# Performance work log

Hardware: AMD Instinct MI355X
Metric: run time of the kernel (lower is better)

Reference implementation:

```python
import jax, jax.numpy as jnp
import numpy as np
import math

HEAD_DIM = 128
DEPTH = 12
LAMBDA_INIT = 0.8 - 0.6 * math.exp(-0.3 * DEPTH)
EPS = 1e-5
SCALE = 1.0 / math.sqrt(HEAD_DIM / 2)


def setup_inputs() -> dict:
    key = jax.random.key(0)
    ks = jax.random.split(key, 8)
    b, t, d = 2, 4096, 2048
    return {
        "x": jax.random.normal(ks[0], (b, t, d), dtype=jnp.float32),
        "wq": jax.random.normal(ks[1], (d, HEAD_DIM), dtype=jnp.float32) * 0.02,
        "wk": jax.random.normal(ks[2], (d, HEAD_DIM), dtype=jnp.float32) * 0.02,
        "wv": jax.random.normal(ks[3], (d, HEAD_DIM), dtype=jnp.float32) * 0.02,
        "lambda_q1": jax.random.normal(ks[4], (HEAD_DIM // 2,), dtype=jnp.float32) * 0.1,
        "lambda_q2": jax.random.normal(ks[5], (HEAD_DIM // 2,), dtype=jnp.float32) * 0.1,
        "lambda_k1": jax.random.normal(ks[6], (HEAD_DIM // 2,), dtype=jnp.float32) * 0.1,
        "lambda_k2": jax.random.normal(ks[7], (HEAD_DIM // 2,), dtype=jnp.float32) * 0.1,
        "ln_weight": jnp.ones((HEAD_DIM,), dtype=jnp.float32),
    }


def reference(x, wq, wk, wv, lambda_q1, lambda_q2, lambda_k1, lambda_k2, ln_weight):
    b, t, d = x.shape
    q = x @ wq  # [b,t,hd]
    k = x @ wk
    v = x @ wv
    h = HEAD_DIM // 2
    q1, q2 = q[..., :h], q[..., h:]
    k1, k2 = k[..., :h], k[..., h:]
    # causal mask: True where attention is disallowed (strictly upper triangle)
    causal = jnp.triu(jnp.ones((t, t), dtype=bool), k=1)
    neg_inf = jnp.float32(-jnp.inf)

    def masked_softmax(qh, kh):
        scores = jnp.einsum('btd,bsd->bts', qh, kh) * SCALE
        scores = jnp.where(causal, neg_inf, scores)
        return jax.nn.softmax(scores, axis=-1)

    a1 = masked_softmax(q1, k1)
    a2 = masked_softmax(q2, k2)
    lmbda = (jnp.exp(jnp.sum(lambda_q1 * lambda_k1))
             - jnp.exp(jnp.sum(lambda_q2 * lambda_k2))
             + LAMBDA_INIT)
    diffattn = jnp.einsum('bts,bsd->btd', a1 - lmbda * a2, v)
    rms = jnp.sqrt(jnp.mean(diffattn * diffattn, axis=-1, keepdims=True) + EPS)
    out = (1.0 - LAMBDA_INIT) * (diffattn / rms * ln_weight)
    return out
```

## Files before the change

kernel.cpp:

```cpp
#include <hip/hip_runtime.h>
#include <stdint.h>

#define T_SEQ 4096
#define NB 2
#define D_MODEL 2048
#define HD 128

typedef __attribute__((ext_vector_type(4)))  float f32x4;
typedef __attribute__((ext_vector_type(16))) float f32x16;
typedef __attribute__((ext_vector_type(8)))  short bf16x8;
typedef __attribute__((ext_vector_type(4)))  unsigned u32x4;

#define LAMBDA_INIT 0.7836057665316244f
#define OUT_SCALE   0.21639423346837556f

__device__ __forceinline__ unsigned short f2bf(float f) {
  unsigned int u = __float_as_uint(f);
  u += 0x7FFFu + ((u >> 16) & 1u);
  return (unsigned short)(u >> 16);
}
__device__ __forceinline__ float bf2f(unsigned short h) {
  return __uint_as_float(((unsigned int)h) << 16);
}
__device__ __forceinline__ unsigned cvt_pk_bf16(float a, float b) {
  unsigned r;
  asm("v_cvt_pk_bf16_f32 %0, %1, %2" : "=v"(r) : "v"(a), "v"(b));
  return r;
}

__global__ __launch_bounds__(256) void qkv_proj(
    const float* __restrict__ x, const float* __restrict__ wq,
    const float* __restrict__ wk, const float* __restrict__ wv,
    unsigned short* __restrict__ qb, unsigned short* __restrict__ kS,
    unsigned short* __restrict__ vS)
{
  __shared__ __align__(16) unsigned short Ah[64 * 4 * 8];
  __shared__ __align__(16) unsigned short Bh[4 * 132 * 8];
  const int which = blockIdx.y;
  const float* w = (which == 0) ? wq : ((which == 1) ? wk : wv);
  const int m0 = blockIdx.x * 64;
  const int tid = threadIdx.x;
  const int lane = tid & 63, wid = tid >> 6;
  const int wm = wid >> 1, wn = wid & 1;
  const int fr = lane & 15, fq = lane >> 4;

  f32x4 acc[2][4];
  #pragma unroll
  for (int i = 0; i < 2; ++i)
    #pragma unroll
    for (int j = 0; j < 4; ++j) acc[i][j] = (f32x4){0.f, 0.f, 0.f, 0.f};

  f32x4 arg[2], brg[4];
  #pragma unroll
  for (int c = 0; c < 2; ++c) {
    int id = tid + c * 256, r = id >> 3, c4 = (id & 7) << 2;
    arg[c] = *reinterpret_cast<const f32x4*>(&x[(size_t)(m0 + r) * D_MODEL + c4]);
  }
  #pragma unroll
  for (int c = 0; c < 4; ++c) {
    int id = tid + c * 256, n = id & 127, kc = (id >> 7) << 2;
    #pragma unroll
    for (int j = 0; j < 4; ++j) brg[c][j] = w[(size_t)(kc + j) * HD + n];
  }

  for (int it = 0; it < 64; ++it) {
    #pragma unroll
    for (int c = 0; c < 2; ++c) {
      int id = tid + c * 256, r = id >> 3, ac = (id & 7) << 2;
      uint2 ph;
      ph.x = cvt_pk_bf16(arg[c][0], arg[c][1]);
      ph.y = cvt_pk_bf16(arg[c][2], arg[c][3]);
      *reinterpret_cast<uint2*>(&Ah[(r * 4 + (ac >> 3)) * 8 + (ac & 4)]) = ph;
    }
    #pragma unroll
    for (int c = 0; c < 4; ++c) {
      int id = tid + c * 256, n = id & 127, kc = (id >> 7) << 2;
      uint2 ph;
      ph.x = cvt_pk_bf16(brg[c][0], brg[c][1]);
      ph.y = cvt_pk_bf16(brg[c][2], brg[c][3]);
      *reinterpret_cast<uint2*>(&Bh[((kc >> 3) * 132 + n) * 8 + (kc & 4)]) = ph;
    }
    __syncthreads();
    if (it < 63) {
      int k0n = (it + 1) * 32;
      #pragma unroll
      for (int c = 0; c < 2; ++c) {
        int id = tid + c * 256, r = id >> 3, c4 = (id & 7) << 2;
        arg[c] = *reinterpret_cast<const f32x4*>(&x[(size_t)(m0 + r) * D_MODEL + k0n + c4]);
      }
      #pragma unroll
      for (int c = 0; c < 4; ++c) {
        int id = tid + c * 256, n = id & 127, kc = (id >> 7) << 2;
        #pragma unroll
        for (int j = 0; j < 4; ++j) brg[c][j] = w[(size_t)(k0n + kc + j) * HD + n];
      }
    }
    bf16x8 ah[2], bh[4];
    #pragma unroll
    for (int mi = 0; mi < 2; ++mi)
      ah[mi] = *reinterpret_cast<bf16x8*>(&Ah[((wm * 32 + mi * 16 + fr) * 4 + fq) * 8]);
    #pragma unroll
    for (int ni = 0; ni < 4; ++ni)
      bh[ni] = *reinterpret_cast<bf16x8*>(&Bh[(fq * 132 + wn * 64 + ni * 16 + fr) * 8]);
    #pragma unroll
    for (int mi = 0; mi < 2; ++mi)
      #pragma unroll
      for (int ni = 0; ni < 4; ++ni)
        acc[mi][ni] = __builtin_amdgcn_mfma_f32_16x16x32_bf16(ah[mi], bh[ni], acc[mi][ni], 0, 0, 0);
    __syncthreads();
  }
  #pragma unroll
  for (int mi = 0; mi < 2; ++mi)
    #pragma unroll
    for (int ni = 0; ni < 4; ++ni) {
      int n = wn * 64 + ni * 16 + fr;
      #pragma unroll
      for (int r = 0; r < 4; ++r) {
        int m = m0 + wm * 32 + mi * 16 + fq * 4 + r;
        float vv = acc[mi][ni][r];
        int bb = m >> 12, tt = m & 4095;
        int kt = tt >> 5, kvl = tt & 31;
        if (which == 0) {
          qb[(size_t)m * HD + n] = f2bf(vv * 0.125f);
        } else if (which == 1) {
          int g = n >> 6, hl = n & 63;
          int ks = hl >> 4, r8 = (hl >> 3) & 1, e = hl & 7;
          size_t idx = ((((((size_t)bb * 128 + kt) * 2 + g) * 4) + ks) << 9)
                     + (size_t)(kvl + 32 * r8) * 8 + e;
          kS[idx] = f2bf(vv);
        } else {
          int f = kvl >> 4, r8 = (kvl >> 3) & 1, e = kvl & 7;
          int vcb = n >> 5;
          size_t idx = (((((size_t)bb * 128 + kt) * 8) + vcb * 2 + f) << 9)
                     + (size_t)((n & 31) + 32 * r8) * 8 + e;
          vS[idx] = f2bf(vv);
        }
      }
    }
}

template<int LOG2S>
__global__ __launch_bounds__(256, 2) void diff_attn_part(
    const unsigned short* __restrict__ qb, const unsigned short* __restrict__ kS,
    const unsigned short* __restrict__ vS,
    unsigned short* __restrict__ po, float* __restrict__ pm, float* __restrict__ pl)
{
  constexpr int S = 1 << LOG2S;
  const int tid = threadIdx.x, lane = tid & 63, wid = tid >> 6;
  const int wave_id = blockIdx.x * 4 + wid;
  const int sp = wave_id & (S - 1);
  const int g  = (wave_id >> LOG2S) & 1;
  const int qt_raw = (wave_id >> (LOG2S + 1)) & 127;
  const int b  = wave_id >> (LOG2S + 8);
  const int qt = 127 - qt_raw;
  const int slot = (((b * 128 + qt) * 2 + g) << LOG2S) + sp;
  const int lq = lane & 31, lh = lane >> 5;
  const int q0 = qt * 32;
  const int n  = qt + 1;
  const int kt0 = (n * sp) >> LOG2S;
  const int kt1 = (n * (sp + 1)) >> LOG2S;

  bf16x8 qf[4];
  const unsigned short* qp = qb + ((size_t)b * T_SEQ + q0 + lq) * HD + g * 64 + lh * 8;
  #pragma unroll
  for (int ks = 0; ks < 4; ++ks) qf[ks] = *reinterpret_cast<const bf16x8*>(qp + ks * 16);

  f32x16 acc[4];
  #pragma unroll
  for (int v = 0; v < 4; ++v)
    #pragma unroll
    for (int r = 0; r < 16; ++r) acc[v][r] = 0.f;
  float mrun = -1e30f, lrun = 0.f;

  const unsigned short* kbase = kS + ((size_t)(b * 128) * 2 + g) * 4 * 512 + lane * 8;
  const unsigned short* vbase = vS + (size_t)(b * 128) * 8 * 512 + lane * 8;
  #define KFRAG(kt, ks) (kbase + ((size_t)(kt) * 8 + (ks)) * 512)
  #define VFRAG(kt, f)  (vbase + ((size_t)(kt) * 8 + (f)) * 512)

  bf16x8 kf[4];
  if (kt0 < kt1) {
    #pragma unroll
    for (int ks = 0; ks < 4; ++ks)
      kf[ks] = *reinterpret_cast<const bf16x8*>(KFRAG(kt0, ks));
  }

  for (int kt = kt0; kt < kt1; ++kt) {
    bf16x8 vfa[4], vfb[4];
    #pragma unroll
    for (int vcb = 0; vcb < 4; ++vcb) {
      vfa[vcb] = *reinterpret_cast<const bf16x8*>(VFRAG(kt, vcb * 2));
      vfb[vcb] = *reinterpret_cast<const bf16x8*>(VFRAG(kt, vcb * 2 + 1));
    }
    bf16x8 kfn[4];
    const bool more = (kt + 1 < kt1);
    if (more) {
      #pragma unroll
      for (int ks = 0; ks < 4; ++ks)
        kfn[ks] = *reinterpret_cast<const bf16x8*>(KFRAG(kt + 1, ks));
    }
    f32x16 sc;
    #pragma unroll
    for (int r = 0; r < 16; ++r) sc[r] = 0.f;
    #pragma unroll
    for (int ks = 0; ks < 4; ++ks)
      sc = __builtin_amdgcn_mfma_f32_32x32x16_bf16(kf[ks], qf[ks], sc, 0, 0, 0);

    float p[16];
    if (kt == n - 1) {
      #pragma unroll
      for (int r = 0; r < 16; ++r) {
        int rloc = (r & 3) + 8 * (r >> 2) + 4 * lh;
        p[r] = (rloc > lq) ? -1e30f : sc[r];
      }
    } else {
      #pragma unroll
      for (int r = 0; r < 16; ++r) p[r] = sc[r];
    }
    float t16[16];
    #pragma unroll
    for (int r = 0; r < 16; ++r) t16[r] = p[r];
    #pragma unroll
    for (int st = 8; st >= 1; st >>= 1)
      #pragma unroll
      for (int r = 0; r < 8; ++r)
        if (r < st) t16[r] = fmaxf(t16[r], t16[r + st]);
    float pmax = fmaxf(t16[0], __shfl_xor(t16[0], 32));
    if (__any(pmax > mrun + 8.f)) {
      float mn = fmaxf(mrun, pmax);
      float al = __expf(mrun - mn);
      lrun *= al;
      #pragma unroll
      for (int v = 0; v < 4; ++v)
        #pragma unroll
        for (int r = 0; r < 16; ++r) acc[v][r] *= al;
      mrun = mn;
    }
    float psum;
    {
      float s16[16];
      #pragma unroll
      for (int r = 0; r < 16; ++r) { p[r] = __expf(p[r] - mrun); s16[r] = p[r]; }
      #pragma unroll
      for (int st = 8; st >= 1; st >>= 1)
        #pragma unroll
        for (int r = 0; r < 8; ++r)
          if (r < st) s16[r] += s16[r + st];
      psum = s16[0];
    }
    lrun += psum + __shfl_xor(psum, 32);

    unsigned A0 = cvt_pk_bf16(p[0],  p[1]),  A1 = cvt_pk_bf16(p[2],  p[3]);
    unsigned A2 = cvt_pk_bf16(p[4],  p[5]),  A3 = cvt_pk_bf16(p[6],  p[7]);
    unsigned A4 = cvt_pk_bf16(p[8],  p[9]),  A5 = cvt_pk_bf16(p[10], p[11]);
    unsigned A6 = cvt_pk_bf16(p[12], p[13]), A7 = cvt_pk_bf16(p[14], p[15]);
    unsigned pA0 = (unsigned)__shfl_xor((int)A0, 32);
    unsigned pA1 = (unsigned)__shfl_xor((int)A1, 32);
    unsigned pA2 = (unsigned)__shfl_xor((int)A2, 32);
    unsigned pA3 = (unsigned)__shfl_xor((int)A3, 32);
    unsigned pA4 = (unsigned)__shfl_xor((int)A4, 32);
    unsigned pA5 = (unsigned)__shfl_xor((int)A5, 32);
    unsigned pA6 = (unsigned)__shfl_xor((int)A6, 32);
    unsigned pA7 = (unsigned)__shfl_xor((int)A7, 32);
    u32x4 w0, w1;
    w0[0] = lh ? pA2 : A0;  w0[1] = lh ? pA3 : A1;
    w0[2] = lh ? A2  : pA0; w0[3] = lh ? A3  : pA1;
    w1[0] = lh ? pA6 : A4;  w1[1] = lh ? pA7 : A5;
    w1[2] = lh ? A6  : pA4; w1[3] = lh ? A7  : pA5;
    bf16x8 pb0 = *reinterpret_cast<bf16x8*>(&w0);
    bf16x8 pb1 = *reinterpret_cast<bf16x8*>(&w1);
    #pragma unroll
    for (int vcb = 0; vcb < 4; ++vcb) {
      acc[vcb] = __builtin_amdgcn_mfma_f32_32x32x16_bf16(vfa[vcb], pb0, acc[vcb], 0, 0, 0);
      acc[vcb] = __builtin_amdgcn_mfma_f32_32x32x16_bf16(vfb[vcb], pb1, acc[vcb], 0, 0, 0);
    }
    if (more) {
      #pragma unroll
      for (int ks = 0; ks < 4; ++ks) kf[ks] = kfn[ks];
    }
  }
  #undef KFRAG
  #undef VFRAG
  const size_t pbase = (size_t)slot * (HD * 32);
  #pragma unroll
  for (int vcb = 0; vcb < 4; ++vcb)
    #pragma unroll
    for (int r = 0; r < 16; ++r) {
      int vc = vcb * 32 + (r & 3) + 8 * (r >> 2) + 4 * lh;
      po[pbase + (size_t)vc * 32 + lq] = f2bf(acc[vcb][r]);
    }
  if (lane < 32) {
    pm[slot * 32 + lq] = mrun;
    pl[slot * 32 + lq] = lrun;
  }
}

template<int LOG2S>
__global__ __launch_bounds__(256) void diff_merge(
    const unsigned short* __restrict__ po, const float* __restrict__ pm,
    const float* __restrict__ pl,
    const float* __restrict__ lq1, const float* __restrict__ lq2,
    const float* __restrict__ lk1, const float* __restrict__ lk2,
    const float* __restrict__ lnw, float* __restrict__ out)
{
  constexpr int S = 1 << LOG2S;
  __shared__ float red[4][32];
  const int tid = threadIdx.x, lane = tid & 63, wid = tid >> 6;
  const int q = tid & 31, vg = tid >> 5;
  const int bq = blockIdx.x;
  const int b = bq >> 7, qt = bq & 127;

  float la = lq1[lane] * lk1[lane];
  float lb = lq2[lane] * lk2[lane];
  #pragma unroll
  for (int off = 32; off >= 1; off >>= 1) {
    la += __shfl_xor(la, off);
    lb += __shfl_xor(lb, off);
  }
  const float lam = __expf(la) - __expf(lb) + LAMBDA_INIT;

  const int p1 = (bq * 2 + 0) * S;
  const int p2 = (bq * 2 + 1) * S;
  float w1[S], w2[S];
  {
    float ms[S];
    #pragma unroll
    for (int s = 0; s < S; ++s) ms[s] = pm[(p1 + s) * 32 + q];
    float M = ms[0];
    #pragma unroll
    for (int s = 1; s < S; ++s) M = fmaxf(M, ms[s]);
    float L = 0.f;
    #pragma unroll
    for (int s = 0; s < S; ++s) { w1[s] = __expf(ms[s] - M); L += w1[s] * pl[(p1 + s) * 32 + q]; }
    float inv = 1.f / L;
    #pragma unroll
    for (int s = 0; s < S; ++s) w1[s] *= inv;
  }
  {
    float ms[S];
    #pragma unroll
    for (int s = 0; s < S; ++s) ms[s] = pm[(p2 + s) * 32 + q];
    float M = ms[0];
    #pragma unroll
    for (int s = 1; s < S; ++s) M = fmaxf(M, ms[s]);
    float L = 0.f;
    #pragma unroll
    for (int s = 0; s < S; ++s) { w2[s] = __expf(ms[s] - M); L += w2[s] * pl[(p2 + s) * 32 + q]; }
    float inv = lam / L;
    #pragma unroll
    for (int s = 0; s < S; ++s) w2[s] *= inv;
  }
  float d[16], ss = 0.f;
  #pragma unroll
  for (int i = 0; i < 16; ++i) {
    int vc = vg * 16 + i;
    float a1 = 0.f, a2 = 0.f;
    #pragma unroll
    for (int s = 0; s < S; ++s) {
      a1 += w1[s] * bf2f(po[(size_t)(p1 + s) * (HD * 32) + (size_t)vc * 32 + q]);
      a2 += w2[s] * bf2f(po[(size_t)(p2 + s) * (HD * 32) + (size_t)vc * 32 + q]);
    }
    d[i] = a1 - a2;
    ss += d[i] * d[i];
  }
  ss += __shfl_xor(ss, 32);
  if (lane < 32) red[wid][q] = ss;
  __syncthreads();
  float tot = red[0][q] + red[1][q] + red[2][q] + red[3][q];
  float rinv = 1.f / sqrtf(tot * (1.0f / HD) + 1e-5f);
  float* op = out + ((size_t)b * T_SEQ + qt * 32 + q) * HD + vg * 16;
  #pragma unroll
  for (int i = 0; i < 16; ++i) op[i] = OUT_SCALE * d[i] * rinv * lnw[vg * 16 + i];
}

extern "C" void kernel_launch(void* const* d_in, const int* in_sizes, int n_in,
                              void* d_out, int out_size, void* d_ws, size_t ws_size,
                              hipStream_t stream) {
  const float* x   = (const float*)d_in[0];
  const float* wq  = (const float*)d_in[1];
  const float* wk  = (const float*)d_in[2];
  const float* wv  = (const float*)d_in[3];
  const float* lq1 = (const float*)d_in[4];
  const float* lq2 = (const float*)d_in[5];
  const float* lk1 = (const float*)d_in[6];
  const float* lk2 = (const float*)d_in[7];
  const float* lnw = (const float*)d_in[8];
  float* out = (float*)d_out;

  const size_t N = (size_t)NB * T_SEQ * HD;
  int log2S = 3;
  for (; log2S > 0; --log2S) {
    size_t parts = ((size_t)NB * 128 * 2) << log2S;
    size_t need = 3 * N * 2 + parts * (HD * 32) * 2 + parts * 32 * 8;
    if (need <= ws_size) break;
  }
  const size_t parts = ((size_t)NB * 128 * 2) << log2S;

  unsigned short* qb = (unsigned short*)d_ws;
  unsigned short* kS = qb + N;
  unsigned short* vS = kS + N;
  unsigned short* po = vS + N;
  float* pm = (float*)(po + parts * (HD * 32));
  float* pl = pm + parts * 32;

  qkv_proj<<<dim3(128, 3), 256, 0, stream>>>(x, wq, wk, wv, qb, kS, vS);
  const int ablocks = (int)(parts / 4);
  switch (log2S) {
    case 3:
      diff_attn_part<3><<<dim3(ablocks), 256, 0, stream>>>(qb, kS, vS, po, pm, pl);
      diff_merge<3><<<dim3(NB * 128), 256, 0, stream>>>(po, pm, pl, lq1, lq2, lk1, lk2, lnw, out);
      break;
    case 2:
      diff_attn_part<2><<<dim3(ablocks), 256, 0, stream>>>(qb, kS, vS, po, pm, pl);
      diff_merge<2><<<dim3(NB * 128), 256, 0, stream>>>(po, pm, pl, lq1, lq2, lk1, lk2, lnw, out);
      break;
    case 1:
      diff_attn_part<1><<<dim3(ablocks), 256, 0, stream>>>(qb, kS, vS, po, pm, pl);
      diff_merge<1><<<dim3(NB * 128), 256, 0, stream>>>(po, pm, pl, lq1, lq2, lk1, lk2, lnw, out);
      break;
    default:
      diff_attn_part<0><<<dim3(ablocks), 256, 0, stream>>>(qb, kS, vS, po, pm, pl);
      diff_merge<0><<<dim3(NB * 128), 256, 0, stream>>>(po, pm, pl, lq1, lq2, lk1, lk2, lnw, out);
      break;
  }
}
```

Baseline: 87.65 us.

## Pretranspose weights to bf16 and double-buffer QKV projection with direct LDS loads

Adds a small kernel that converts the three weight matrices to bf16 in an MFMA-friendly layout, folding the query scale into the weights. The projection GEMM then streams weight tiles straight into LDS with global_load_lds, double-buffers both operands, and doubles the K-step per iteration to 64, halving the barrier count. This removes the strided scalar fp32 weight loads and per-iteration conversions from the GEMM loop. In exchange it adds an extra launch, extra workspace, and more LDS per block, which lowers occupancy.

```diff
diff --git a/kernel.cpp b/kernel.cpp
--- a/kernel.cpp
+++ b/kernel.cpp
@@ -27,86 +27,127 @@
   asm("v_cvt_pk_bf16_f32 %0, %1, %2" : "=v"(r) : "v"(a), "v"(b));
   return r;
 }
-
-__global__ __launch_bounds__(256) void qkv_proj(
-    const float* __restrict__ x, const float* __restrict__ wq,
-    const float* __restrict__ wk, const float* __restrict__ wv,
+__device__ __forceinline__ void gload16(const void* g, void* l) {
+  __builtin_amdgcn_global_load_lds(
+      (const __attribute__((address_space(1))) unsigned int*)g,
+      (__attribute__((address_space(3))) unsigned int*)l, 16, 0, 0);
+}
+
+__global__ __launch_bounds__(256) void wtrans(
+    const float* __restrict__ wq, const float* __restrict__ wk,
+    const float* __restrict__ wv, unsigned short* __restrict__ wT)
+{
+  const int which = blockIdx.y;
+  const int s = blockIdx.x;
+  const float* w = (which == 0) ? wq : ((which == 1) ? wk : wv);
+  const float scale = (which == 0) ? 0.125f : 1.0f;
+  const int tid = threadIdx.x;
+  #pragma unroll
+  for (int j = 0; j < 4; ++j) {
+    int cell = j * 256 + tid;
+    int q = cell >> 7, n = cell & 127;
+    int kb = s * 64 + q * 8;
+    float v[8];
+    #pragma unroll
+    for (int e = 0; e < 8; ++e) v[e] = w[(size_t)(kb + e) * HD + n] * scale;
+    u32x4 pk = { cvt_pk_bf16(v[0], v[1]), cvt_pk_bf16(v[2], v[3]),
+                 cvt_pk_bf16(v[4], v[5]), cvt_pk_bf16(v[6], v[7]) };
+    *reinterpret_cast<u32x4*>(&wT[(size_t)(which * 32 + s) * 8192 + (size_t)cell * 8]) = pk;
+  }
+}
+
+__global__ __launch_bounds__(256, 2) void qkv_proj(
+    const float* __restrict__ x, const unsigned short* __restrict__ wT,
     unsigned short* __restrict__ qb, unsigned short* __restrict__ kS,
     unsigned short* __restrict__ vS)
 {
-  __shared__ __align__(16) unsigned short Ah[64 * 4 * 8];
-  __shared__ __align__(16) unsigned short Bh[4 * 132 * 8];
+  __shared__ __align__(16) unsigned short Ab[2][4096];
+  __shared__ __align__(16) unsigned short Bb[2][8192];
   const int which = blockIdx.y;
-  const float* w = (which == 0) ? wq : ((which == 1) ? wk : wv);
   const int m0 = blockIdx.x * 64;
   const int tid = threadIdx.x;
   const int lane = tid & 63, wid = tid >> 6;
   const int wm = wid >> 1, wn = wid & 1;
   const int fr = lane & 15, fq = lane >> 4;
 
+  const unsigned short* wslab = wT + (size_t)which * 32 * 8192;
+
+  const int arow = tid & 31, aq = tid >> 5;
+  const float* xa = x + (size_t)(m0 + arow) * D_MODEL + aq * 8;
+  const float* xb = xa + (size_t)32 * D_MODEL;
+
   f32x4 acc[2][4];
   #pragma unroll
   for (int i = 0; i < 2; ++i)
     #pragma unroll
     for (int j = 0; j < 4; ++j) acc[i][j] = (f32x4){0.f, 0.f, 0.f, 0.f};
 
-  f32x4 arg[2], brg[4];
-  #pragma unroll
-  for (int c = 0; c < 2; ++c) {
-    int id = tid + c * 256, r = id >> 3, c4 = (id & 7) << 2;
-    arg[c] = *reinterpret_cast<const f32x4*>(&x[(size_t)(m0 + r) * D_MODEL + c4]);
-  }
-  #pragma unroll
-  for (int c = 0; c < 4; ++c) {
-    int id = tid + c * 256, n = id & 127, kc = (id >> 7) << 2;
-    #pragma unroll
-    for (int j = 0; j < 4; ++j) brg[c][j] = w[(size_t)(kc + j) * HD + n];
-  }
-
-  for (int it = 0; it < 64; ++it) {
-    #pragma unroll
-    for (int c = 0; c < 2; ++c) {
-      int id = tid + c * 256, r = id >> 3, ac = (id & 7) << 2;
-      uint2 ph;
-      ph.x = cvt_pk_bf16(arg[c][0], arg[c][1]);
-      ph.y = cvt_pk_bf16(arg[c][2], arg[c][3]);
-      *reinterpret_cast<uint2*>(&Ah[(r * 4 + (ac >> 3)) * 8 + (ac & 4)]) = ph;
-    }
-    #pragma unroll
-    for (int c = 0; c < 4; ++c) {
-      int id = tid + c * 256, n = id & 127, kc = (id >> 7) << 2;
-      uint2 ph;
-      ph.x = cvt_pk_bf16(brg[c][0], brg[c][1]);
-      ph.y = cvt_pk_bf16(brg[c][2], brg[c][3]);
-      *reinterpret_cast<uint2*>(&Bh[((kc >> 3) * 132 + n) * 8 + (kc & 4)]) = ph;
-    }
-    __syncthreads();
-    if (it < 63) {
-      int k0n = (it + 1) * 32;
-      #pragma unroll
-      for (int c = 0; c < 2; ++c) {
-        int id = tid + c * 256, r = id >> 3, c4 = (id & 7) << 2;
-        arg[c] = *reinterpret_cast<const f32x4*>(&x[(size_t)(m0 + r) * D_MODEL + k0n + c4]);
+  {
+    f32x4 u0 = *reinterpret_cast<const f32x4*>(xa);
+    f32x4 u1 = *reinterpret_cast<const f32x4*>(xa + 4);
+    f32x4 u2 = *reinterpret_cast<const f32x4*>(xb);
+    f32x4 u3 = *reinterpret_cast<const f32x4*>(xb + 4);
+    u32x4 c0 = { cvt_pk_bf16(u0[0], u0[1]), cvt_pk_bf16(u0[2], u0[3]),
+                 cvt_pk_bf16(u1[0], u1[1]), cvt_pk_bf16(u1[2], u1[3]) };
+    u32x4 c1 = { cvt_pk_bf16(u2[0], u2[1]), cvt_pk_bf16(u2[2], u2[3]),
+                 cvt_pk_bf16(u3[0], u3[1]), cvt_pk_bf16(u3[2], u3[3]) };
+    *reinterpret_cast<u32x4*>(&Ab[0][(size_t)(aq * 64 + arow) * 8]) = c0;
+    *reinterpret_cast<u32x4*>(&Ab[0][(size_t)(aq * 64 + arow + 32) * 8]) = c1;
+    #pragma unroll
+    for (int j = 0; j < 4; ++j) {
+      int ch = wid * 4 + j;
+      gload16(wslab + (size_t)ch * 512 + (size_t)lane * 8, (char*)&Bb[0][ch * 512]);
+    }
+  }
+  f32x4 a0 = *reinterpret_cast<const f32x4*>(xa + 64);
+  f32x4 a1 = *reinterpret_cast<const f32x4*>(xa + 68);
+  f32x4 a2 = *reinterpret_cast<const f32x4*>(xb + 64);
+  f32x4 a3 = *reinterpret_cast<const f32x4*>(xb + 68);
+  __syncthreads();
+
+  for (int it = 0; it < 32; ++it) {
+    const int cur = it & 1;
+    if (it < 31) {
+      #pragma unroll
+      for (int j = 0; j < 4; ++j) {
+        int ch = wid * 4 + j;
+        gload16(wslab + (size_t)(it + 1) * 8192 + (size_t)ch * 512 + (size_t)lane * 8,
+                (char*)&Bb[cur ^ 1][ch * 512]);
       }
-      #pragma unroll
-      for (int c = 0; c < 4; ++c) {
-        int id = tid + c * 256, n = id & 127, kc = (id >> 7) << 2;
+      u32x4 c0 = { cvt_pk_bf16(a0[0], a0[1]), cvt_pk_bf16(a0[2], a0[3]),
+                   cvt_pk_bf16(a1[0], a1[1]), cvt_pk_bf16(a1[2], a1[3]) };
+      u32x4 c1 = { cvt_pk_bf16(a2[0], a2[1]), cvt_pk_bf16(a2[2], a2[3]),
+                   cvt_pk_bf16(a3[0], a3[1]), cvt_pk_bf16(a3[2], a3[3]) };
+      *reinterpret_cast<u32x4*>(&Ab[cur ^ 1][(size_t)(aq * 64 + arow) * 8]) = c0;
+      *reinterpret_cast<u32x4*>(&Ab[cur ^ 1][(size_t)(aq * 64 + arow + 32) * 8]) = c1;
+      if (it < 30) {
+        const int kn = (it + 2) * 64;
+        a0 = *reinterpret_cast<const f32x4*>(xa + kn);
+        a1 = *reinterpret_cast<const f32x4*>(xa + kn + 4);
+        a2 = *reinterpret_cast<const f32x4*>(xb + kn);
+        a3 = *reinterpret_cast<const f32x4*>(xb + kn + 4);
+      }
+    }
+    bf16x8 ah[2][2], bh[2][4];
+    #pragma unroll
+    for (int mi = 0; mi < 2; ++mi) {
+      int row = wm * 32 + mi * 16 + fr;
+      ah[mi][0] = *reinterpret_cast<bf16x8*>(&Ab[cur][(size_t)(fq * 64 + row) * 8]);
+      ah[mi][1] = *reinterpret_cast<bf16x8*>(&Ab[cur][(size_t)((4 + fq) * 64 + row) * 8]);
+    }
+    #pragma unroll
+    for (int ni = 0; ni < 4; ++ni) {
+      int nrow = wn * 64 + ni * 16 + fr;
+      bh[0][ni] = *reinterpret_cast<bf16x8*>(&Bb[cur][(size_t)(fq * 128 + nrow) * 8]);
+      bh[1][ni] = *reinterpret_cast<bf16x8*>(&Bb[cur][(size_t)((4 + fq) * 128 + nrow) * 8]);
+    }
+    #pragma unroll
+    for (int kk = 0; kk < 2; ++kk)
+      #pragma unroll
+      for (int mi = 0; mi < 2; ++mi)
         #pragma unroll
-        for (int j = 0; j < 4; ++j) brg[c][j] = w[(size_t)(k0n + kc + j) * HD + n];
-      }
-    }
-    bf16x8 ah[2], bh[4];
-    #pragma unroll
-    for (int mi = 0; mi < 2; ++mi)
-      ah[mi] = *reinterpret_cast<bf16x8*>(&Ah[((wm * 32 + mi * 16 + fr) * 4 + fq) * 8]);
-    #pragma unroll
-    for (int ni = 0; ni < 4; ++ni)
-      bh[ni] = *reinterpret_cast<bf16x8*>(&Bh[(fq * 132 + wn * 64 + ni * 16 + fr) * 8]);
-    #pragma unroll
-    for (int mi = 0; mi < 2; ++mi)
-      #pragma unroll
-      for (int ni = 0; ni < 4; ++ni)
-        acc[mi][ni] = __builtin_amdgcn_mfma_f32_16x16x32_bf16(ah[mi], bh[ni], acc[mi][ni], 0, 0, 0);
+        for (int ni = 0; ni < 4; ++ni)
+          acc[mi][ni] = __builtin_amdgcn_mfma_f32_16x16x32_bf16(ah[mi][kk], bh[kk][ni], acc[mi][ni], 0, 0, 0);
     __syncthreads();
   }
   #pragma unroll
@@ -121,7 +162,7 @@
         int bb = m >> 12, tt = m & 4095;
         int kt = tt >> 5, kvl = tt & 31;
         if (which == 0) {
-          qb[(size_t)m * HD + n] = f2bf(vv * 0.125f);
+          qb[(size_t)m * HD + n] = f2bf(vv);
         } else if (which == 1) {
           int g = n >> 6, hl = n & 63;
           int ks = hl >> 4, r8 = (hl >> 3) & 1, e = hl & 7;
@@ -387,10 +428,11 @@
   float* out = (float*)d_out;
 
   const size_t N = (size_t)NB * T_SEQ * HD;
+  const size_t WTN = (size_t)3 * 32 * 8192;
   int log2S = 3;
   for (; log2S > 0; --log2S) {
     size_t parts = ((size_t)NB * 128 * 2) << log2S;
-    size_t need = 3 * N * 2 + parts * (HD * 32) * 2 + parts * 32 * 8;
+    size_t need = 3 * N * 2 + WTN * 2 + parts * (HD * 32) * 2 + parts * 32 * 8;
     if (need <= ws_size) break;
   }
   const size_t parts = ((size_t)NB * 128 * 2) << log2S;
@@ -398,11 +440,13 @@
   unsigned short* qb = (unsigned short*)d_ws;
   unsigned short* kS = qb + N;
   unsigned short* vS = kS + N;
-  unsigned short* po = vS + N;
+  unsigned short* wT = vS + N;
+  unsigned short* po = wT + WTN;
   float* pm = (float*)(po + parts * (HD * 32));
   float* pl = pm + parts * 32;
 
-  qkv_proj<<<dim3(128, 3), 256, 0, stream>>>(x, wq, wk, wv, qb, kS, vS);
+  wtrans<<<dim3(32, 3), 256, 0, stream>>>(wq, wk, wv, wT);
+  qkv_proj<<<dim3(128, 3), 256, 0, stream>>>(x, wT, qb, kS, vS);
   const int ablocks = (int)(parts / 4);
   switch (log2S) {
     case 3:
```

After: 97.90 us. 1.12x slower.
